# Kernel tuning notes

Measured on AMD Instinct MI355X. Metric: run time of the kernel, lower is better.

Reference implementation:

```python
import jax, jax.numpy as jnp
import numpy as np

WS = 8            # window_size
N = WS * WS       # tokens per window = 64
C = 512           # dim
TEMB = 512        # temb_dim
H = 8             # num_heads
D = C // H        # head_dim = 64
B = 2048          # number of windows (batch * windows per image)


def _rel_pos_index(ws: int) -> np.ndarray:
    coords = np.stack(np.meshgrid(np.arange(ws), np.arange(ws), indexing='ij'))  # (2, ws, ws)
    flat = coords.reshape(2, -1)                      # (2, N)
    rel = flat[:, :, None] - flat[:, None, :]         # (2, N, N)
    rel = rel.transpose(1, 2, 0).copy()               # (N, N, 2)
    rel[:, :, 0] += ws - 1
    rel[:, :, 1] += ws - 1
    rel[:, :, 0] *= 2 * ws - 1
    return rel.sum(-1)                                # (N, N) int

_RP_INDEX = jnp.asarray(_rel_pos_index(WS))           # (N, N)


def setup_inputs() -> dict:
    key = jax.random.key(0)
    ks = jax.random.split(key, 8)
    std = 0.02
    return {
        'x': jax.random.normal(ks[0], (B, N, C), dtype=jnp.float32),
        'temb': jax.random.normal(ks[1], (B, TEMB), dtype=jnp.float32),
        'w_qkv': jax.random.normal(ks[2], (C, 3 * C), dtype=jnp.float32) * std,
        'b_qkv': jnp.zeros((3 * C,), dtype=jnp.float32),
        'w_qkv_t': jax.random.normal(ks[3], (TEMB, 3 * C), dtype=jnp.float32) * std,
        'w_proj': jax.random.normal(ks[4], (C, C), dtype=jnp.float32) * std,
        'b_proj': jnp.zeros((C,), dtype=jnp.float32),
        'rpb_table': jax.random.normal(ks[5], ((2 * WS - 1) ** 2, H), dtype=jnp.float32) * std,
    }


def reference(x, temb, w_qkv, b_qkv, w_qkv_t, w_proj, b_proj, rpb_table):
    # x: (B, N, C), temb: (B, TEMB)
    scale = D ** (-0.5)
    qkv = x @ w_qkv + b_qkv + (temb @ w_qkv_t)[:, None, :]     # (B, N, 3C)
    qkv = qkv.reshape(x.shape[0], N, 3, H, D)
    q = qkv[:, :, 0].transpose(0, 2, 1, 3)                      # (B, H, N, D)
    k = qkv[:, :, 1].transpose(0, 2, 1, 3)
    v = qkv[:, :, 2].transpose(0, 2, 1, 3)
    attn = jnp.einsum('bhnd,bhmd->bhnm', q * scale, k)          # (B, H, N, N)
    bias = rpb_table[_RP_INDEX]                                 # (N, N, H)
    attn = attn + bias.transpose(2, 0, 1)[None]                 # + (1, H, N, N)
    attn = jax.nn.softmax(attn, axis=-1)
    out = jnp.einsum('bhnm,bhmd->bhnd', attn, v)                # (B, H, N, D)
    out = out.transpose(0, 2, 1, 3).reshape(x.shape[0], N, C)   # (B, N, C)
    return out @ w_proj + b_proj
```

## Files before the change

kernel.cpp:

```cpp
#include <hip/hip_runtime.h>

typedef __bf16 bf16;
typedef __bf16 bf16x4 __attribute__((ext_vector_type(4)));
typedef __bf16 bf16x8 __attribute__((ext_vector_type(8)));
typedef float f32x4 __attribute__((ext_vector_type(4)));

#define MFMA(a, b, c) __builtin_amdgcn_mfma_f32_16x16x32_bf16((a), (b), (c), 0, 0, 0)

constexpr size_t SEC = (size_t)2048 * 8 * 64 * 64;

template <bool B> struct BC { static constexpr bool v = B; };

__device__ __forceinline__ void gload16(const void* g, void* l) {
  __builtin_amdgcn_global_load_lds((const __attribute__((address_space(1))) void*)g,
                                   (__attribute__((address_space(3))) void*)l, 16, 0, 0);
}

__global__ void transpose_cast(const float* __restrict__ in, bf16* __restrict__ out,
                               int R, int C) {
  int i = blockIdx.x * 256 + threadIdx.x;
  if (i >= R * C) return;
  int r = i / C, c = i - r * C;
  out[(size_t)c * R + r] = (bf16)in[i];
}

__global__ __launch_bounds__(256) void cast_bf16(const float* __restrict__ in,
                                                 bf16* __restrict__ out) {
  size_t i = ((size_t)blockIdx.x * 256 + threadIdx.x) * 8;
  f32x4 v0 = *((const f32x4*)(in + i));
  f32x4 v1 = *((const f32x4*)(in + i + 4));
  bf16x8 pk;
  pk[0] = (bf16)v0[0]; pk[1] = (bf16)v0[1]; pk[2] = (bf16)v0[2]; pk[3] = (bf16)v0[3];
  pk[4] = (bf16)v1[0]; pk[5] = (bf16)v1[1]; pk[6] = (bf16)v1[2]; pk[7] = (bf16)v1[3];
  *((bf16x8*)(out + i)) = pk;
}

__global__ __launch_bounds__(256) void gemm_temb(
    const float* __restrict__ Ap, const bf16* __restrict__ Bt,
    const float* __restrict__ bias, float* __restrict__ C,
    int M, int N, int K) {
  __shared__ bf16 lA[128 * 32];
  __shared__ bf16 lB[128 * 32];
  const int t = threadIdx.x, l = t & 63;
  const int w = t >> 6, wr = w >> 1, wc = w & 1;
  const int li = l & 15, kl = (l >> 4) << 3;
  const long bm0 = (long)blockIdx.x * 128, bn0 = (long)blockIdx.y * 128;
  f32x4 acc[4][4] = {};
  for (int ks = 0; ks < (K >> 5); ++ks) {
    const int k0 = ks << 5;
    __syncthreads();
#pragma unroll
    for (int i = 0; i < 2; ++i) {
      int u = t + (i << 8);
      int row = u >> 2, kc = (u & 3) << 3;
      const float* ag = Ap + (bm0 + row) * K + k0 + kc;
      f32x4 v0 = *((const f32x4*)ag);
      f32x4 v1 = *((const f32x4*)(ag + 4));
      bf16x8 pk;
      pk[0] = (bf16)v0[0]; pk[1] = (bf16)v0[1]; pk[2] = (bf16)v0[2]; pk[3] = (bf16)v0[3];
      pk[4] = (bf16)v1[0]; pk[5] = (bf16)v1[1]; pk[6] = (bf16)v1[2]; pk[7] = (bf16)v1[3];
      *((bf16x8*)&lA[u << 3]) = pk;
      *((bf16x8*)&lB[u << 3]) = *((const bf16x8*)&Bt[(bn0 + row) * K + k0 + kc]);
    }
    __syncthreads();
    bf16x8 af[4], bfr[4];
#pragma unroll
    for (int mt = 0; mt < 4; ++mt)
      af[mt] = *((const bf16x8*)&lA[(wr * 64 + mt * 16 + li) * 32 + kl]);
#pragma unroll
    for (int nt = 0; nt < 4; ++nt)
      bfr[nt] = *((const bf16x8*)&lB[(wc * 64 + nt * 16 + li) * 32 + kl]);
#pragma unroll
    for (int mt = 0; mt < 4; ++mt)
#pragma unroll
      for (int nt = 0; nt < 4; ++nt)
        acc[mt][nt] = MFMA(af[mt], bfr[nt], acc[mt][nt]);
  }
#pragma unroll
  for (int mt = 0; mt < 4; ++mt)
#pragma unroll
    for (int nt = 0; nt < 4; ++nt) {
      long col = bn0 + wc * 64 + nt * 16 + li;
      float bv = bias[col];
#pragma unroll
      for (int r = 0; r < 4; ++r) {
        long row = bm0 + wr * 64 + mt * 16 + ((l >> 4) << 2) + r;
        C[row * N + col] = acc[mt][nt][r] + bv;
      }
    }
}

template <int MODE>
__global__ __launch_bounds__(256) void mm128(
    const void* __restrict__ Ap, const bf16* __restrict__ Bt,
    const float* __restrict__ biasv, void* __restrict__ Cp) {
  __shared__ bf16 lA[3][128 * 32];
  __shared__ bf16 lB[3][128 * 32];
  constexpr int NB = (MODE == 1) ? 12 : 4;
  const int t = threadIdx.x, l = t & 63;
  const int w = t >> 6, wr = w >> 1, wc = w & 1;
  const int li = l & 15, lg = l >> 4;

  const int wg = blockIdx.x;
  const int xcd = wg & 7, idx = wg >> 3;
  const int mb = xcd * 128 + idx / NB;
  const int nb = idx % NB;
  const int bm0 = mb * 128, bnG = nb * 128;
  const bool isv = (MODE == 1) && (bnG >= 1024);

  const int srow = t >> 2, sp = t & 3;

  auto stage = [&](int ks, int buf) {
    const int k0 = ks << 5;
#pragma unroll
    for (int i = 0; i < 2; ++i) {
      int row = srow + (i << 6);
      int c0 = k0 + ((sp ^ ((row >> 1) & 3)) << 3);
      const bf16* asrc;
      if (MODE == 1) {
        asrc = (const bf16*)Ap + (size_t)(bm0 + row) * 512 + c0;
      } else {
        int gr = bm0 + row;
        asrc = (const bf16*)Ap + (((size_t)(gr >> 6) * 8 + (c0 >> 6)) << 12) +
               (gr & 63) * 64 + (c0 & 63);
      }
      gload16(asrc, &lA[buf][(w * 64 + (i << 8)) * 8]);
      gload16(Bt + (size_t)(bnG + row) * 512 + c0, &lB[buf][(w * 64 + (i << 8)) * 8]);
    }
  };

  f32x4 acc[4][4] = {};

  auto kloop = [&](auto swc) {
    constexpr bool SW = decltype(swc)::v;
    stage(0, 0);
    stage(1, 1);
#pragma unroll
    for (int ks = 0; ks < 16; ++ks) {
      if (ks < 15) asm volatile("s_waitcnt vmcnt(4)" ::: "memory");
      else         asm volatile("s_waitcnt vmcnt(0)" ::: "memory");
      __builtin_amdgcn_s_barrier();
      if (ks < 14) stage(ks + 2, (ks + 2) % 3);
      const int cb = ks % 3;
      bf16x8 af[4], bfr[4];
#pragma unroll
      for (int mt = 0; mt < 4; ++mt) {
        int row = wr * 64 + mt * 16 + li;
        af[mt] = *((const bf16x8*)&lA[cb][row * 32 + ((lg ^ ((row >> 1) & 3)) << 3)]);
      }
#pragma unroll
      for (int nt = 0; nt < 4; ++nt) {
        int row = wc * 64 + nt * 16 + li;
        bfr[nt] = *((const bf16x8*)&lB[cb][row * 32 + ((lg ^ ((row >> 1) & 3)) << 3)]);
      }
      __builtin_amdgcn_s_setprio(1);
#pragma unroll
      for (int mt = 0; mt < 4; ++mt)
#pragma unroll
        for (int nt = 0; nt < 4; ++nt)
          acc[mt][nt] = SW ? MFMA(bfr[nt], af[mt], acc[mt][nt])
                           : MFMA(af[mt], bfr[nt], acc[mt][nt]);
      __builtin_amdgcn_s_setprio(0);
    }
  };
  if (isv) kloop(BC<true>{}); else kloop(BC<false>{});

  if (MODE == 0) {
    float* C = (float*)Cp;
#pragma unroll
    for (int nt = 0; nt < 4; ++nt) {
      int col = bnG + wc * 64 + nt * 16 + li;
      float bv = biasv[col];
#pragma unroll
      for (int mt = 0; mt < 4; ++mt) {
        int row = bm0 + wr * 64 + mt * 16 + (lg << 2);
#pragma unroll
        for (int r = 0; r < 4; ++r)
          C[(size_t)(row + r) * 512 + col] = acc[mt][nt][r] + bv;
      }
    }
  } else if (!isv) {
    bf16* qkv = (bf16*)Cp;
    const int b = (bm0 >> 6) + wr;
#pragma unroll
    for (int nt = 0; nt < 4; ++nt) {
      int col = bnG + wc * 64 + nt * 16 + li;
      int sec = col >> 9, h = (col >> 6) & 7, d = col & 63;
      float bv = biasv[(size_t)b * 1536 + col];
      float sc = (sec == 0) ? 0.125f : 1.0f;
      bf16* dst = qkv + (size_t)sec * SEC + (((size_t)b * 8 + h) << 12) + d;
#pragma unroll
      for (int mt = 0; mt < 4; ++mt) {
        int n0 = mt * 16 + (lg << 2);
#pragma unroll
        for (int r = 0; r < 4; ++r)
          dst[(n0 + r) * 64] = (bf16)((acc[mt][nt][r] + bv) * sc);
      }
    }
  } else {
    bf16* qkv = (bf16*)Cp;
    const int b = (bm0 >> 6) + wr;
#pragma unroll
    for (int nt = 0; nt < 4; ++nt) {
      int colb = bnG + wc * 64 + nt * 16 + (lg << 2);
#pragma unroll
      for (int r = 0; r < 4; ++r) {
        int col = colb + r;
        int h = (col >> 6) & 7, d = col & 63;
        float bv = biasv[(size_t)b * 1536 + col];
        bf16* dst = qkv + 2 * SEC + (((size_t)b * 8 + h) << 12) + d * 64;
#pragma unroll
        for (int mt = 0; mt < 4; ++mt) {
          int n = mt * 16 + li;
          dst[n] = (bf16)(acc[mt][nt][r] + bv);
        }
      }
    }
  }
}

__global__ __launch_bounds__(256, 4) void attn_win(bf16* qkv,
                                                   const float* __restrict__ rpb) {
  __shared__ bf16 stg[2][3][4096];
  const int b = blockIdx.x, t = threadIdx.x, l = t & 63, w = t >> 6;
  const int li = l & 15, lg = l >> 4;

  int rpidx[4][4];
#pragma unroll
  for (int ct = 0; ct < 4; ++ct)
#pragma unroll
    for (int r = 0; r < 4; ++r) {
      int n = 16 * w + (lg << 2) + r, m = 16 * ct + li;
      rpidx[ct][r] = (((n >> 3) - (m >> 3) + 7) * 15 + ((n & 7) - (m & 7) + 7)) * 8;
    }

  auto stage = [&](int h, int buf) {
#pragma unroll
    for (int tt = 0; tt < 3; ++tt) {
      const bf16* src = qkv + (size_t)tt * SEC + (((size_t)b * 8 + h) << 12);
#pragma unroll
      for (int i = 0; i < 2; ++i) {
        int u = t + (i << 8);
        int row = u >> 3, s = u & 7;
        gload16(src + row * 64 + ((s ^ (row & 7)) << 3),
                &stg[buf][tt][(w * 64 + (i << 8)) * 8]);
      }
    }
  };

  stage(0, 0);
  for (int h = 0; h < 8; ++h) {
    const int buf = h & 1;
    __syncthreads();
    if (h < 7) stage(h + 1, buf ^ 1);
    bf16* Q = stg[buf][0];
    const bf16* K = stg[buf][1];
    const bf16* V = stg[buf][2];

    f32x4 accS[4] = {};
#pragma unroll
    for (int kk = 0; kk < 2; ++kk) {
      int row = 16 * w + li;
      bf16x8 aq = *((const bf16x8*)&Q[row * 64 + (((kk * 4 + lg) ^ (row & 7)) << 3)]);
#pragma unroll
      for (int ct = 0; ct < 4; ++ct) {
        int kr = 16 * ct + li;
        bf16x8 bk = *((const bf16x8*)&K[kr * 64 + (((kk * 4 + lg) ^ (kr & 7)) << 3)]);
        accS[ct] = MFMA(aq, bk, accS[ct]);
      }
    }
    const float* rpbh = rpb + h;
    float sv[4][4], rsum[4];
#pragma unroll
    for (int ct = 0; ct < 4; ++ct)
#pragma unroll
      for (int r = 0; r < 4; ++r)
        sv[ct][r] = accS[ct][r] + rpbh[rpidx[ct][r]];
#pragma unroll
    for (int r = 0; r < 4; ++r) {
      float m = fmaxf(fmaxf(sv[0][r], sv[1][r]), fmaxf(sv[2][r], sv[3][r]));
      m = fmaxf(m, __shfl_xor(m, 1));
      m = fmaxf(m, __shfl_xor(m, 2));
      m = fmaxf(m, __shfl_xor(m, 4));
      m = fmaxf(m, __shfl_xor(m, 8));
      float s = 0.f;
#pragma unroll
      for (int ct = 0; ct < 4; ++ct) {
        float p = __expf(sv[ct][r] - m);
        sv[ct][r] = p;
        s += p;
      }
      s += __shfl_xor(s, 1);
      s += __shfl_xor(s, 2);
      s += __shfl_xor(s, 4);
      s += __shfl_xor(s, 8);
      rsum[r] = s;
    }
#pragma unroll
    for (int ct = 0; ct < 4; ++ct)
#pragma unroll
      for (int r = 0; r < 4; ++r) {
        int row = 16 * w + (lg << 2) + r;
        int col = 16 * ct + li;
        Q[row * 64 + (((col >> 3) ^ (row & 7)) << 3) + (col & 7)] = (bf16)sv[ct][r];
      }
    f32x4 accO[4] = {};
#pragma unroll
    for (int kk = 0; kk < 2; ++kk) {
      int row = 16 * w + li;
      bf16x8 ap = *((const bf16x8*)&Q[row * 64 + (((kk * 4 + lg) ^ (row & 7)) << 3)]);
#pragma unroll
      for (int ct = 0; ct < 4; ++ct) {
        int vr = 16 * ct + li;
        bf16x8 bv = *((const bf16x8*)&V[vr * 64 + (((kk * 4 + lg) ^ (vr & 7)) << 3)]);
        accO[ct] = MFMA(ap, bv, accO[ct]);
      }
    }
    bf16* ob = qkv + (((size_t)b * 8 + h) << 12);
    float rinv[4];
#pragma unroll
    for (int r = 0; r < 4; ++r) rinv[r] = 1.0f / rsum[r];
#pragma unroll
    for (int ct = 0; ct < 4; ++ct)
#pragma unroll
      for (int r = 0; r < 4; ++r)
        ob[(16 * w + (lg << 2) + r) * 64 + 16 * ct + li] = (bf16)(accO[ct][r] * rinv[r]);
  }
}

extern "C" void kernel_launch(void* const* d_in, const int* in_sizes, int n_in,
                              void* d_out, int out_size, void* d_ws, size_t ws_size,
                              hipStream_t stream) {
  (void)in_sizes; (void)n_in; (void)out_size; (void)ws_size;
  const float* x       = (const float*)d_in[0];
  const float* temb    = (const float*)d_in[1];
  const float* w_qkv   = (const float*)d_in[2];
  const float* b_qkv   = (const float*)d_in[3];
  const float* w_qkv_t = (const float*)d_in[4];
  const float* w_proj  = (const float*)d_in[5];
  const float* b_proj  = (const float*)d_in[6];
  const float* rpb     = (const float*)d_in[7];
  float* out = (float*)d_out;

  char* ws = (char*)d_ws;
  size_t off = 0;
  auto take = [&](size_t bytes) {
    void* p = ws + off;
    off += (bytes + 255) & ~(size_t)255;
    return p;
  };
  bf16* w1t  = (bf16*)take((size_t)1536 * 512 * 2);
  bf16* w3t  = (bf16*)take((size_t)1536 * 512 * 2);
  bf16* w2t  = (bf16*)take((size_t)512 * 512 * 2);
  float* tb  = (float*)take((size_t)2048 * 1536 * 4);
  bf16* qkv  = (bf16*)take(3 * SEC * 2);
  bf16* xb   = (bf16*)take((size_t)131072 * 512 * 2);

  transpose_cast<<<(512 * 1536 + 255) / 256, 256, 0, stream>>>(w_qkv, w1t, 512, 1536);
  transpose_cast<<<(512 * 1536 + 255) / 256, 256, 0, stream>>>(w_qkv_t, w3t, 512, 1536);
  transpose_cast<<<(512 * 512 + 255) / 256, 256, 0, stream>>>(w_proj, w2t, 512, 512);

  cast_bf16<<<(131072 * 512 / 8) / 256, 256, 0, stream>>>(x, xb);

  gemm_temb<<<dim3(2048 / 128, 1536 / 128), 256, 0, stream>>>(
      temb, w3t, b_qkv, tb, 2048, 1536, 512);

  mm128<1><<<12 * 1024, 256, 0, stream>>>(xb, w1t, tb, qkv);

  attn_win<<<2048, 256, 0, stream>>>(qkv, rpb);

  mm128<0><<<4 * 1024, 256, 0, stream>>>(qkv, w2t, b_proj, out);
}
```

Measured before the change: 761.4 us.

## Make GEMM blocks own a full row strip and loop over all N tiles

The QKV and projection GEMMs now launch one workgroup per 128-row strip, and each workgroup iterates over every 128-column tile. The three-buffer LDS load pipeline runs continuously across tile boundaries, so the next tile's loads overlap the current tile's epilogue stores. The A strip is re-read by the same workgroup, which may improve cache locality. In exchange, far fewer workgroups run (1024), the loop is no longer fully unrolled, the epilogue branch is chosen at runtime, and the setprio hints are dropped.

After: 1.078 ms. 1.42x slower.

```diff
diff --git a/kernel.cpp b/kernel.cpp
--- a/kernel.cpp
+++ b/kernel.cpp
@@ -8,8 +8,6 @@
 #define MFMA(a, b, c) __builtin_amdgcn_mfma_f32_16x16x32_bf16((a), (b), (c), 0, 0, 0)
 
 constexpr size_t SEC = (size_t)2048 * 8 * 64 * 64;
-
-template <bool B> struct BC { static constexpr bool v = B; };
 
 __device__ __forceinline__ void gload16(const void* g, void* l) {
   __builtin_amdgcn_global_load_lds((const __attribute__((address_space(1))) void*)g,
@@ -91,26 +89,27 @@
 }
 
 template <int MODE>
-__global__ __launch_bounds__(256) void mm128(
+__global__ __launch_bounds__(256) void mm_pers(
     const void* __restrict__ Ap, const bf16* __restrict__ Bt,
     const float* __restrict__ biasv, void* __restrict__ Cp) {
   __shared__ bf16 lA[3][128 * 32];
   __shared__ bf16 lB[3][128 * 32];
   constexpr int NB = (MODE == 1) ? 12 : 4;
+  constexpr int S = 16 * NB;
   const int t = threadIdx.x, l = t & 63;
   const int w = t >> 6, wr = w >> 1, wc = w & 1;
   const int li = l & 15, lg = l >> 4;
 
   const int wg = blockIdx.x;
   const int xcd = wg & 7, idx = wg >> 3;
-  const int mb = xcd * 128 + idx / NB;
-  const int nb = idx % NB;
-  const int bm0 = mb * 128, bnG = nb * 128;
-  const bool isv = (MODE == 1) && (bnG >= 1024);
+  const int mb = xcd * 128 + idx;
+  const int bm0 = mb * 128;
+  const int b = (bm0 >> 6) + wr;
 
   const int srow = t >> 2, sp = t & 3;
 
-  auto stage = [&](int ks, int buf) {
+  auto stage = [&](int s2, int buf) {
+    const int ks = s2 & 15, nb = s2 >> 4;
     const int k0 = ks << 5;
 #pragma unroll
     for (int i = 0; i < 2; ++i) {
@@ -125,23 +124,26 @@
                (gr & 63) * 64 + (c0 & 63);
       }
       gload16(asrc, &lA[buf][(w * 64 + (i << 8)) * 8]);
-      gload16(Bt + (size_t)(bnG + row) * 512 + c0, &lB[buf][(w * 64 + (i << 8)) * 8]);
+      gload16(Bt + (size_t)(nb * 128 + row) * 512 + c0,
+              &lB[buf][(w * 64 + (i << 8)) * 8]);
     }
   };
 
   f32x4 acc[4][4] = {};
-
-  auto kloop = [&](auto swc) {
-    constexpr bool SW = decltype(swc)::v;
-    stage(0, 0);
-    stage(1, 1);
-#pragma unroll
+  stage(0, 0);
+  stage(1, 1);
+  int cb = 0, sb = 2;
+
+  for (int nb = 0; nb < NB; ++nb) {
     for (int ks = 0; ks < 16; ++ks) {
-      if (ks < 15) asm volatile("s_waitcnt vmcnt(4)" ::: "memory");
-      else         asm volatile("s_waitcnt vmcnt(0)" ::: "memory");
+      const int s = nb * 16 + ks;
+      if (s < S - 1) asm volatile("s_waitcnt vmcnt(4)" ::: "memory");
+      else           asm volatile("s_waitcnt vmcnt(0)" ::: "memory");
       __builtin_amdgcn_s_barrier();
-      if (ks < 14) stage(ks + 2, (ks + 2) % 3);
-      const int cb = ks % 3;
+      if (s < S - 2) {
+        stage(s + 2, sb);
+        sb = (sb == 2) ? 0 : sb + 1;
+      }
       bf16x8 af[4], bfr[4];
 #pragma unroll
       for (int mt = 0; mt < 4; ++mt) {
@@ -153,69 +155,77 @@
         int row = wc * 64 + nt * 16 + li;
         bfr[nt] = *((const bf16x8*)&lB[cb][row * 32 + ((lg ^ ((row >> 1) & 3)) << 3)]);
       }
-      __builtin_amdgcn_s_setprio(1);
-#pragma unroll
-      for (int mt = 0; mt < 4; ++mt)
-#pragma unroll
-        for (int nt = 0; nt < 4; ++nt)
-          acc[mt][nt] = SW ? MFMA(bfr[nt], af[mt], acc[mt][nt])
-                           : MFMA(af[mt], bfr[nt], acc[mt][nt]);
-      __builtin_amdgcn_s_setprio(0);
-    }
-  };
-  if (isv) kloop(BC<true>{}); else kloop(BC<false>{});
-
-  if (MODE == 0) {
-    float* C = (float*)Cp;
-#pragma unroll
-    for (int nt = 0; nt < 4; ++nt) {
-      int col = bnG + wc * 64 + nt * 16 + li;
-      float bv = biasv[col];
-#pragma unroll
-      for (int mt = 0; mt < 4; ++mt) {
-        int row = bm0 + wr * 64 + mt * 16 + (lg << 2);
-#pragma unroll
-        for (int r = 0; r < 4; ++r)
-          C[(size_t)(row + r) * 512 + col] = acc[mt][nt][r] + bv;
-      }
-    }
-  } else if (!isv) {
-    bf16* qkv = (bf16*)Cp;
-    const int b = (bm0 >> 6) + wr;
-#pragma unroll
-    for (int nt = 0; nt < 4; ++nt) {
-      int col = bnG + wc * 64 + nt * 16 + li;
-      int sec = col >> 9, h = (col >> 6) & 7, d = col & 63;
-      float bv = biasv[(size_t)b * 1536 + col];
-      float sc = (sec == 0) ? 0.125f : 1.0f;
-      bf16* dst = qkv + (size_t)sec * SEC + (((size_t)b * 8 + h) << 12) + d;
-#pragma unroll
-      for (int mt = 0; mt < 4; ++mt) {
-        int n0 = mt * 16 + (lg << 2);
-#pragma unroll
-        for (int r = 0; r < 4; ++r)
-          dst[(n0 + r) * 64] = (bf16)((acc[mt][nt][r] + bv) * sc);
-      }
-    }
-  } else {
-    bf16* qkv = (bf16*)Cp;
-    const int b = (bm0 >> 6) + wr;
-#pragma unroll
-    for (int nt = 0; nt < 4; ++nt) {
-      int colb = bnG + wc * 64 + nt * 16 + (lg << 2);
-#pragma unroll
-      for (int r = 0; r < 4; ++r) {
-        int col = colb + r;
-        int h = (col >> 6) & 7, d = col & 63;
+      if (MODE == 1 && nb >= 8) {
+#pragma unroll
+        for (int mt = 0; mt < 4; ++mt)
+#pragma unroll
+          for (int nt = 0; nt < 4; ++nt)
+            acc[mt][nt] = MFMA(bfr[nt], af[mt], acc[mt][nt]);
+      } else {
+#pragma unroll
+        for (int mt = 0; mt < 4; ++mt)
+#pragma unroll
+          for (int nt = 0; nt < 4; ++nt)
+            acc[mt][nt] = MFMA(af[mt], bfr[nt], acc[mt][nt]);
+      }
+      cb = (cb == 2) ? 0 : cb + 1;
+    }
+
+    if (MODE == 0) {
+      float* C = (float*)Cp;
+#pragma unroll
+      for (int nt = 0; nt < 4; ++nt) {
+        int col = nb * 128 + wc * 64 + nt * 16 + li;
+        float bv = biasv[col];
+#pragma unroll
+        for (int mt = 0; mt < 4; ++mt) {
+          int row = bm0 + wr * 64 + mt * 16 + (lg << 2);
+#pragma unroll
+          for (int r = 0; r < 4; ++r)
+            C[(size_t)(row + r) * 512 + col] = acc[mt][nt][r] + bv;
+        }
+      }
+    } else if (nb < 8) {
+      bf16* qkv = (bf16*)Cp;
+#pragma unroll
+      for (int nt = 0; nt < 4; ++nt) {
+        int col = nb * 128 + wc * 64 + nt * 16 + li;
+        int sec = col >> 9, h = (col >> 6) & 7, d = col & 63;
         float bv = biasv[(size_t)b * 1536 + col];
-        bf16* dst = qkv + 2 * SEC + (((size_t)b * 8 + h) << 12) + d * 64;
+        float sc = (sec == 0) ? 0.125f : 1.0f;
+        bf16* dst = qkv + (size_t)sec * SEC + (((size_t)b * 8 + h) << 12) + d;
 #pragma unroll
         for (int mt = 0; mt < 4; ++mt) {
-          int n = mt * 16 + li;
-          dst[n] = (bf16)(acc[mt][nt][r] + bv);
+          int n0 = mt * 16 + (lg << 2);
+#pragma unroll
+          for (int r = 0; r < 4; ++r)
+            dst[(n0 + r) * 64] = (bf16)((acc[mt][nt][r] + bv) * sc);
         }
       }
-    }
+    } else {
+      bf16* qkv = (bf16*)Cp;
+#pragma unroll
+      for (int nt = 0; nt < 4; ++nt) {
+        int colb = nb * 128 + wc * 64 + nt * 16 + (lg << 2);
+#pragma unroll
+        for (int r = 0; r < 4; ++r) {
+          int col = colb + r;
+          int h = (col >> 6) & 7, d = col & 63;
+          float bv = biasv[(size_t)b * 1536 + col];
+          bf16* dst = qkv + 2 * SEC + (((size_t)b * 8 + h) << 12) + d * 64;
+#pragma unroll
+          for (int mt = 0; mt < 4; ++mt) {
+            int n = mt * 16 + li;
+            dst[n] = (bf16)(acc[mt][nt][r] + bv);
+          }
+        }
+      }
+    }
+#pragma unroll
+    for (int mt = 0; mt < 4; ++mt)
+#pragma unroll
+      for (int nt = 0; nt < 4; ++nt)
+        acc[mt][nt] = (f32x4){0.f, 0.f, 0.f, 0.f};
   }
 }
 
@@ -365,9 +375,9 @@
   gemm_temb<<<dim3(2048 / 128, 1536 / 128), 256, 0, stream>>>(
       temb, w3t, b_qkv, tb, 2048, 1536, 512);
 
-  mm128<1><<<12 * 1024, 256, 0, stream>>>(xb, w1t, tb, qkv);
+  mm_pers<1><<<1024, 256, 0, stream>>>(xb, w1t, tb, qkv);
 
   attn_win<<<2048, 256, 0, stream>>>(qkv, rpb);
 
-  mm128<0><<<4 * 1024, 256, 0, stream>>>(qkv, w2t, b_proj, out);
-}
+  mm_pers<0><<<1024, 256, 0, stream>>>(qkv, w2t, b_proj, out);
+}
```
